# Optimization experiments

Measured on AMD Instinct MI355X. Metric: run time of the kernel, lower is better.

## Reference

```python
import jax, jax.numpy as jnp
import numpy as np

NUM_USERS = 100000
NUM_ITEMS = 100000
DIM = 128
B = 8192
H = 200
ATTN_HID = 64


def setup_inputs() -> dict:
    key = jax.random.key(0)
    ks = jax.random.split(key, 10)
    user_ids = jax.random.randint(ks[0], (B,), 0, NUM_USERS)
    item_ids = jax.random.randint(ks[1], (B,), 0, NUM_ITEMS)
    user_history = jax.random.randint(ks[2], (B, H), 0, NUM_ITEMS)
    user_table = jax.random.normal(ks[3], (NUM_USERS, DIM), dtype=jnp.float32)
    item_table = jax.random.normal(ks[4], (NUM_ITEMS, DIM), dtype=jnp.float32)
    feature_interaction = jax.random.normal(ks[5], (DIM, DIM), dtype=jnp.float32)
    # attention MLP: Linear(2*DIM, 64) -> ReLU -> Linear(64, 1) -> Sigmoid
    lim1 = 1.0 / np.sqrt(2 * DIM)
    w1 = jax.random.uniform(ks[6], (2 * DIM, ATTN_HID), minval=-lim1, maxval=lim1, dtype=jnp.float32)
    b1 = jax.random.uniform(ks[7], (ATTN_HID,), minval=-lim1, maxval=lim1, dtype=jnp.float32)
    lim2 = 1.0 / np.sqrt(ATTN_HID)
    w2 = jax.random.uniform(ks[8], (ATTN_HID, 1), minval=-lim2, maxval=lim2, dtype=jnp.float32)
    b2 = jax.random.uniform(ks[9], (1,), minval=-lim2, maxval=lim2, dtype=jnp.float32)
    return {
        "user_ids": user_ids,
        "item_ids": item_ids,
        "user_history": user_history,
        "user_table": user_table,
        "item_table": item_table,
        "feature_interaction": feature_interaction,
        "w1": w1,
        "b1": b1,
        "w2": w2,
        "b2": b2,
    }


def reference(user_ids, item_ids, user_history, user_table, item_table,
              feature_interaction, w1, b1, w2, b2):
    user_emb = user_table[user_ids]          # [B, D]
    item_emb = item_table[item_ids]          # [B, D]
    # bilinear interaction: (user_emb @ W) . item_emb, summed over D -> [B, 1]
    interaction = jnp.sum((user_emb @ feature_interaction) * item_emb, axis=1, keepdims=True)
    # attention-weighted history pooling
    history_emb = item_table[user_history]   # [B, H, D]
    u = jnp.broadcast_to(user_emb[:, None, :], history_emb.shape)  # [B, H, D]
    attn_in = jnp.concatenate([u, history_emb], axis=-1)           # [B, H, 2D]
    h = jax.nn.relu(attn_in @ w1 + b1)                             # [B, H, 64]
    attn_w = jax.nn.sigmoid(h @ w2 + b2)                           # [B, H, 1]
    history_repr = jnp.sum(attn_w * history_emb, axis=1)           # [B, D]
    user_out = user_emb + history_repr
    return (user_out, item_emb, interaction)
```

## Files before the change

kernel.cpp:

```cpp
#include <hip/hip_runtime.h>
#include <math.h>

#define NB      8192
#define HLEN    200
#define DIM     128
#define AH      64
#define NITEMS  100000
#define NTILE   13

typedef __attribute__((ext_vector_type(4))) float f32x4;
typedef __attribute__((ext_vector_type(2))) float f32x2;
typedef __attribute__((ext_vector_type(4))) int   i32x4;
typedef __attribute__((ext_vector_type(8))) short bf16x8;

__device__ __forceinline__ unsigned short f2bf(float f) {
  unsigned int u = __float_as_uint(f);
  u += 0x7fffu + ((u >> 16) & 1u);
  return (unsigned short)(u >> 16);
}
__device__ __forceinline__ float bf2f(unsigned short h) {
  return __uint_as_float(((unsigned int)h) << 16);
}
__device__ __forceinline__ long pick64(const i32x4& v, int h) {
  return (long)(unsigned)v[2 * h] | ((long)(unsigned)v[2 * h + 1] << 32);
}

__global__ void convert_kernel(const float* __restrict__ tbl,
                               const float* __restrict__ w1,
                               unsigned char* __restrict__ tbl8,
                               unsigned char* __restrict__ w1f8) {
  const long total4 = (long)NITEMS * DIM / 4;
  const long stride = (long)gridDim.x * blockDim.x;
  const long t0 = (long)blockIdx.x * blockDim.x + threadIdx.x;
  for (long i = t0; i < total4; i += stride) {
    f32x4 v = ((const f32x4*)tbl)[i];
    int p = __builtin_amdgcn_cvt_pk_fp8_f32(v[0], v[1], 0, false);
    p     = __builtin_amdgcn_cvt_pk_fp8_f32(v[2], v[3], p, true);
    ((int*)tbl8)[i] = p;
  }
  if (t0 < 16384) {
    int L = (int)t0;
    int j  = L & 7, gg = (L >> 3) & 3, mm = (L >> 5) & 15;
    int nt = (L >> 9) & 3, s = (L >> 11) & 3, part = (L >> 13) & 1;
    int kg = part * 128 + (s >> 1) * 64 + gg * 16 + (s & 1) * 8 + j;
    int n  = nt * 16 + mm;
    float v = w1[kg * AH + n];
    int p = __builtin_amdgcn_cvt_pk_fp8_f32(v, v, 0, false);
    w1f8[L] = (unsigned char)(p & 0xff);
  }
}

__global__ __launch_bounds__(256)
void main_kernel_fp8(const int* __restrict__ user_ids,
                     const int* __restrict__ user_history,
                     const float* __restrict__ user_table,
                     const unsigned char* __restrict__ tbl8,
                     const unsigned char* __restrict__ w1f8,
                     const float* __restrict__ b1,
                     const float* __restrict__ w2,
                     const float* __restrict__ b2,
                     float* __restrict__ out_user) {
  const int lane = threadIdx.x & 63;
  const int wave = threadIdx.x >> 6;
  const int b = blockIdx.x * 4 + wave;
  const int m = lane & 15;
  const int g = lane >> 4;

  const int uid = __builtin_amdgcn_readfirstlane(user_ids[b]);
  const float* urow = user_table + (long)uid * DIM;
  const int* hrow = user_history + (long)b * HLEN;

  int idxs[NTILE];
#pragma unroll
  for (int t = 0; t < NTILE; ++t) {
    int row = t * 16 + m;
    idxs[t] = (row < HLEN) ? hrow[row] : 0;
  }

  i32x4 uf[2];
#pragma unroll
  for (int kb = 0; kb < 2; ++kb) {
    const float* up = urow + kb * 64 + g * 16;
    f32x4 q0 = *(const f32x4*)(up + 0);
    f32x4 q1 = *(const f32x4*)(up + 4);
    f32x4 q2 = *(const f32x4*)(up + 8);
    f32x4 q3 = *(const f32x4*)(up + 12);
    i32x4 d;
    d[0] = __builtin_amdgcn_cvt_pk_fp8_f32(q0[0], q0[1], 0, false);
    d[0] = __builtin_amdgcn_cvt_pk_fp8_f32(q0[2], q0[3], d[0], true);
    d[1] = __builtin_amdgcn_cvt_pk_fp8_f32(q1[0], q1[1], 0, false);
    d[1] = __builtin_amdgcn_cvt_pk_fp8_f32(q1[2], q1[3], d[1], true);
    d[2] = __builtin_amdgcn_cvt_pk_fp8_f32(q2[0], q2[1], 0, false);
    d[2] = __builtin_amdgcn_cvt_pk_fp8_f32(q2[2], q2[3], d[2], true);
    d[3] = __builtin_amdgcn_cvt_pk_fp8_f32(q3[0], q3[1], 0, false);
    d[3] = __builtin_amdgcn_cvt_pk_fp8_f32(q3[2], q3[3], d[3], true);
    uf[kb] = d;
  }

  const unsigned char* wtop = w1f8;
  const unsigned char* wbot = w1f8 + 8192;

  f32x4 accu[4];
#pragma unroll
  for (int nt = 0; nt < 4; ++nt) accu[nt] = (f32x4){0.f, 0.f, 0.f, 0.f};
#pragma unroll
  for (int s = 0; s < 4; ++s) {
    long a_s = pick64(uf[s >> 1], s & 1);
#pragma unroll
    for (int nt = 0; nt < 4; ++nt) {
      long bf = *(const long*)(wtop + ((s * 4 + nt) * 16 + m) * 32 + g * 8);
      accu[nt] = __builtin_amdgcn_mfma_f32_16x16x32_fp8_fp8(a_s, bf, accu[nt], 0, 0, 0);
    }
  }
  float ubreg[4], w2reg[4];
#pragma unroll
  for (int nt = 0; nt < 4; ++nt) {
    ubreg[nt] = accu[nt][0] + b1[nt * 16 + m];
    w2reg[nt] = w2[nt * 16 + m];
  }
  const float b2v = b2[0];

  long bfr[4][4];
#pragma unroll
  for (int s = 0; s < 4; ++s)
#pragma unroll
    for (int nt = 0; nt < 4; ++nt)
      bfr[s][nt] = *(const long*)(wbot + ((s * 4 + nt) * 16 + m) * 32 + g * 8);

  float arep[32];
#pragma unroll
  for (int c = 0; c < 32; ++c) arep[c] = 0.f;

  i32x4 pa[3][2];
#define LOADT(T, BUF)                                                          \
  {                                                                            \
    const unsigned char* p_ = tbl8 + ((long)idxs[T] << 7) + g * 16;            \
    pa[BUF][0] = *(const i32x4*)p_;                                            \
    pa[BUF][1] = *(const i32x4*)(p_ + 64);                                     \
  }
  LOADT(0, 0)
  LOADT(1, 1)
#pragma unroll
  for (int t = 0; t < NTILE; ++t) {
    if (t + 2 < NTILE) LOADT(t + 2, (t + 2) % 3)
    const int cb = t % 3;

    f32x4 acc[4];
#pragma unroll
    for (int nt = 0; nt < 4; ++nt) acc[nt] = (f32x4){0.f, 0.f, 0.f, 0.f};
#pragma unroll
    for (int s = 0; s < 4; ++s) {
      long a_s = pick64(pa[cb][s >> 1], s & 1);
#pragma unroll
      for (int nt = 0; nt < 4; ++nt)
        acc[nt] = __builtin_amdgcn_mfma_f32_16x16x32_fp8_fp8(a_s, bfr[s][nt], acc[nt], 0, 0, 0);
    }

    float sums[4];
#pragma unroll
    for (int r = 0; r < 4; ++r) {
      float s = 0.f;
#pragma unroll
      for (int nt = 0; nt < 4; ++nt) {
        float h = fmaxf(acc[nt][r] + ubreg[nt], 0.f);
        s = fmaf(h, w2reg[nt], s);
      }
      s += __shfl_xor(s, 1);
      s += __shfl_xor(s, 2);
      s += __shfl_xor(s, 4);
      s += __shfl_xor(s, 8);
      sums[r] = s;
    }
    const int q = m & 3;
    float keep = (q == 0) ? sums[0] : (q == 1) ? sums[1] : (q == 2) ? sums[2] : sums[3];
    float sv = __shfl(keep, ((m >> 2) << 4) | m);
    float attw = 1.f / (1.f + __expf(-(sv + b2v)));
    if (t * 16 + m >= HLEN) attw = 0.f;

#pragma unroll
    for (int kb = 0; kb < 2; ++kb)
#pragma unroll
      for (int d = 0; d < 4; ++d) {
        f32x2 lo = __builtin_amdgcn_cvt_pk_f32_fp8(pa[cb][kb][d], false);
        f32x2 hi = __builtin_amdgcn_cvt_pk_f32_fp8(pa[cb][kb][d], true);
        const int base = kb * 16 + d * 4;
        arep[base + 0] = fmaf(attw, lo[0], arep[base + 0]);
        arep[base + 1] = fmaf(attw, lo[1], arep[base + 1]);
        arep[base + 2] = fmaf(attw, hi[0], arep[base + 2]);
        arep[base + 3] = fmaf(attw, hi[1], arep[base + 3]);
      }
  }
#undef LOADT

#pragma unroll
  for (int c = 0; c < 32; ++c) {
    arep[c] += __shfl_xor(arep[c], 1);
    arep[c] += __shfl_xor(arep[c], 2);
    arep[c] += __shfl_xor(arep[c], 4);
    arep[c] += __shfl_xor(arep[c], 8);
  }
  if (m == 0) {
#pragma unroll
    for (int kb = 0; kb < 2; ++kb)
#pragma unroll
      for (int i4 = 0; i4 < 4; ++i4) {
        const int col = kb * 64 + g * 16 + i4 * 4;
        f32x4 uv = *(const f32x4*)(urow + col);
        f32x4 o;
#pragma unroll
        for (int qq = 0; qq < 4; ++qq) o[qq] = uv[qq] + arep[kb * 16 + i4 * 4 + qq];
        *(f32x4*)(out_user + (long)b * DIM + col) = o;
      }
  }
}

__global__ __launch_bounds__(256)
void main_fallback(const int* __restrict__ user_ids,
                   const int* __restrict__ user_history,
                   const float* __restrict__ user_table,
                   const float* __restrict__ item_table,
                   const float* __restrict__ w1,
                   const float* __restrict__ b1,
                   const float* __restrict__ w2,
                   const float* __restrict__ b2,
                   float* __restrict__ out_user) {
  const int lane = threadIdx.x & 63;
  const int wave = threadIdx.x >> 6;
  const int b = blockIdx.x * 4 + wave;
  const int m = lane & 15, g = lane >> 4;
  const int uid = __builtin_amdgcn_readfirstlane(user_ids[b]);
  const float* urow = user_table + (long)uid * DIM;
  float upj = b1[lane];
#pragma unroll 8
  for (int d = 0; d < DIM; ++d) upj = fmaf(urow[d], w1[d * AH + lane], upj);
  bf16x8 bfr[4][4];
#pragma unroll
  for (int ks = 0; ks < 4; ++ks)
#pragma unroll
    for (int nt = 0; nt < 4; ++nt) {
      bf16x8 bv;
#pragma unroll
      for (int j = 0; j < 8; ++j)
        bv[j] = (short)f2bf(w1[(DIM + ks * 32 + g * 8 + j) * AH + nt * 16 + m]);
      bfr[ks][nt] = bv;
    }
  float ubreg[4], w2reg[4];
#pragma unroll
  for (int nt = 0; nt < 4; ++nt) {
    ubreg[nt] = __shfl(upj, nt * 16 + m);
    w2reg[nt] = w2[nt * 16 + m];
  }
  const float b2v = b2[0];
  float arep[32];
#pragma unroll
  for (int c = 0; c < 32; ++c) arep[c] = 0.f;
  const int* hrow = user_history + (long)b * HLEN;
  for (int t = 0; t < NTILE; ++t) {
    const int row = t * 16 + m;
    const int idx = (row < HLEN) ? hrow[row] : 0;
    bf16x8 a[4];
    const float* rp = item_table + (long)idx * DIM;
#pragma unroll
    for (int ks = 0; ks < 4; ++ks) {
      f32x4 lo = *(const f32x4*)(rp + ks * 32 + g * 8);
      f32x4 hi = *(const f32x4*)(rp + ks * 32 + g * 8 + 4);
      bf16x8 av;
      av[0] = (short)f2bf(lo[0]); av[1] = (short)f2bf(lo[1]);
      av[2] = (short)f2bf(lo[2]); av[3] = (short)f2bf(lo[3]);
      av[4] = (short)f2bf(hi[0]); av[5] = (short)f2bf(hi[1]);
      av[6] = (short)f2bf(hi[2]); av[7] = (short)f2bf(hi[3]);
      a[ks] = av;
    }
    f32x4 acc[4];
#pragma unroll
    for (int nt = 0; nt < 4; ++nt) acc[nt] = (f32x4){0.f, 0.f, 0.f, 0.f};
#pragma unroll
    for (int ks = 0; ks < 4; ++ks)
#pragma unroll
      for (int nt = 0; nt < 4; ++nt)
        acc[nt] = __builtin_amdgcn_mfma_f32_16x16x32_bf16(a[ks], bfr[ks][nt], acc[nt], 0, 0, 0);
    float sums[4];
#pragma unroll
    for (int r = 0; r < 4; ++r) {
      float s = 0.f;
#pragma unroll
      for (int nt = 0; nt < 4; ++nt) {
        float h = fmaxf(acc[nt][r] + ubreg[nt], 0.f);
        s = fmaf(h, w2reg[nt], s);
      }
      s += __shfl_xor(s, 1); s += __shfl_xor(s, 2);
      s += __shfl_xor(s, 4); s += __shfl_xor(s, 8);
      sums[r] = s;
    }
    const int q = m & 3;
    float keep = (q == 0) ? sums[0] : (q == 1) ? sums[1] : (q == 2) ? sums[2] : sums[3];
    float sv = __shfl(keep, ((m >> 2) << 4) | m);
    float attw = 1.f / (1.f + __expf(-(sv + b2v)));
    if (row >= HLEN) attw = 0.f;
#pragma unroll
    for (int ks = 0; ks < 4; ++ks)
#pragma unroll
      for (int j = 0; j < 8; ++j)
        arep[ks * 8 + j] = fmaf(attw, bf2f((unsigned short)a[ks][j]), arep[ks * 8 + j]);
  }
#pragma unroll
  for (int c = 0; c < 32; ++c) {
    arep[c] += __shfl_xor(arep[c], 1);
    arep[c] += __shfl_xor(arep[c], 2);
    arep[c] += __shfl_xor(arep[c], 4);
    arep[c] += __shfl_xor(arep[c], 8);
  }
  if (m == 0) {
#pragma unroll
    for (int ks = 0; ks < 4; ++ks)
#pragma unroll
      for (int j = 0; j < 8; ++j) {
        const int col = ks * 32 + g * 8 + j;
        out_user[(long)b * DIM + col] = urow[col] + arep[ks * 8 + j];
      }
  }
}

__global__ __launch_bounds__(256, 2)
void inter_kernel(const int* __restrict__ user_ids,
                  const int* __restrict__ item_ids,
                  const float* __restrict__ user_table,
                  const float* __restrict__ item_table,
                  const float* __restrict__ fi,
                  float* __restrict__ out_item,
                  float* __restrict__ out_inter) {
  __shared__ unsigned short fitb[DIM * 130];
  __shared__ float u4[4][DIM];
  __shared__ float red[4][4];
  const int t = threadIdx.x;
  for (int i = t; i < DIM * DIM; i += 256) {
    int d = i >> 7, e = i & 127;
    fitb[e * 130 + d] = f2bf(fi[i]);
  }
  const int col = t & 127;
  const int dh = t >> 7;
  const int lane = t & 63;
  const int wv = t >> 6;
  const int b0 = blockIdx.x * 32;
  const unsigned short* fr = &fitb[col * 130 + dh * 64];

  for (int grp = 0; grp < 8; ++grp) {
    __syncthreads();
    for (int i = t; i < 4 * DIM; i += 256) {
      int bi = i >> 7, d = i & 127;
      u4[bi][d] = user_table[(long)user_ids[b0 + grp * 4 + bi] * DIM + d];
    }
    __syncthreads();
    float a0 = 0.f, a1 = 0.f, a2 = 0.f, a3 = 0.f;
#pragma unroll 4
    for (int d = 0; d < 64; d += 4) {
      float f0 = bf2f(fr[d]), f1 = bf2f(fr[d + 1]), f2 = bf2f(fr[d + 2]), f3 = bf2f(fr[d + 3]);
      f32x4 q0 = *(const f32x4*)&u4[0][dh * 64 + d];
      f32x4 q1 = *(const f32x4*)&u4[1][dh * 64 + d];
      f32x4 q2 = *(const f32x4*)&u4[2][dh * 64 + d];
      f32x4 q3 = *(const f32x4*)&u4[3][dh * 64 + d];
      a0 = fmaf(f0, q0[0], a0); a0 = fmaf(f1, q0[1], a0); a0 = fmaf(f2, q0[2], a0); a0 = fmaf(f3, q0[3], a0);
      a1 = fmaf(f0, q1[0], a1); a1 = fmaf(f1, q1[1], a1); a1 = fmaf(f2, q1[2], a1); a1 = fmaf(f3, q1[3], a1);
      a2 = fmaf(f0, q2[0], a2); a2 = fmaf(f1, q2[1], a2); a2 = fmaf(f2, q2[2], a2); a2 = fmaf(f3, q2[3], a2);
      a3 = fmaf(f0, q3[0], a3); a3 = fmaf(f1, q3[1], a3); a3 = fmaf(f2, q3[2], a3); a3 = fmaf(f3, q3[3], a3);
    }
    const int bb = b0 + grp * 4;
    const float vv0 = item_table[(long)item_ids[bb + 0] * DIM + col];
    const float vv1 = item_table[(long)item_ids[bb + 1] * DIM + col];
    const float vv2 = item_table[(long)item_ids[bb + 2] * DIM + col];
    const float vv3 = item_table[(long)item_ids[bb + 3] * DIM + col];
    if (dh == 0) {
      out_item[(long)(bb + 0) * DIM + col] = vv0;
      out_item[(long)(bb + 1) * DIM + col] = vv1;
      out_item[(long)(bb + 2) * DIM + col] = vv2;
      out_item[(long)(bb + 3) * DIM + col] = vv3;
    }
    float p0 = a0 * vv0, p1 = a1 * vv1, p2 = a2 * vv2, p3 = a3 * vv3;
#pragma unroll
    for (int msk = 1; msk <= 32; msk <<= 1) {
      p0 += __shfl_xor(p0, msk);
      p1 += __shfl_xor(p1, msk);
      p2 += __shfl_xor(p2, msk);
      p3 += __shfl_xor(p3, msk);
    }
    if (lane == 0) { red[wv][0] = p0; red[wv][1] = p1; red[wv][2] = p2; red[wv][3] = p3; }
    __syncthreads();
    if (t < 4)
      out_inter[bb + t] = red[0][t] + red[1][t] + red[2][t] + red[3][t];
  }
}

extern "C" void kernel_launch(void* const* d_in, const int* in_sizes, int n_in,
                              void* d_out, int out_size, void* d_ws, size_t ws_size,
                              hipStream_t stream) {
  const int*   user_ids     = (const int*)d_in[0];
  const int*   item_ids     = (const int*)d_in[1];
  const int*   user_history = (const int*)d_in[2];
  const float* user_table   = (const float*)d_in[3];
  const float* item_table   = (const float*)d_in[4];
  const float* fi           = (const float*)d_in[5];
  const float* w1           = (const float*)d_in[6];
  const float* b1           = (const float*)d_in[7];
  const float* w2           = (const float*)d_in[8];
  const float* b2           = (const float*)d_in[9];

  float* out       = (float*)d_out;
  float* out_user  = out;
  float* out_item  = out + (size_t)NB * DIM;
  float* out_inter = out + (size_t)2 * NB * DIM;

  const size_t need = (size_t)NITEMS * DIM + 16384;
  if (ws_size >= need) {
    unsigned char* tbl8 = (unsigned char*)d_ws;
    unsigned char* w1f8 = tbl8 + (size_t)NITEMS * DIM;
    convert_kernel<<<1536, 256, 0, stream>>>(item_table, w1, tbl8, w1f8);
    main_kernel_fp8<<<NB / 4, 256, 0, stream>>>(user_ids, user_history, user_table,
        tbl8, w1f8, b1, w2, b2, out_user);
  } else {
    main_fallback<<<NB / 4, 256, 0, stream>>>(user_ids, user_history, user_table,
        item_table, w1, b1, w2, b2, out_user);
  }
  inter_kernel<<<NB / 32, 256, 0, stream>>>(user_ids, item_ids, user_table, item_table,
        fi, out_item, out_inter);
}
```

Measured before the change: 106.9 us.

## Merge interaction kernel into conversion kernel and deepen gather prefetch

```diff
diff --git a/kernel.cpp b/kernel.cpp
--- a/kernel.cpp
+++ b/kernel.cpp
@@ -7,46 +7,120 @@
 #define AH      64
 #define NITEMS  100000
 #define NTILE   13
+#define INTER_BLKS (NB / 32)
 
 typedef __attribute__((ext_vector_type(4))) float f32x4;
 typedef __attribute__((ext_vector_type(2))) float f32x2;
 typedef __attribute__((ext_vector_type(4))) int   i32x4;
 typedef __attribute__((ext_vector_type(8))) short bf16x8;
+typedef unsigned int uint;
 
 __device__ __forceinline__ unsigned short f2bf(float f) {
-  unsigned int u = __float_as_uint(f);
+  uint u = __float_as_uint(f);
   u += 0x7fffu + ((u >> 16) & 1u);
   return (unsigned short)(u >> 16);
 }
 __device__ __forceinline__ float bf2f(unsigned short h) {
-  return __uint_as_float(((unsigned int)h) << 16);
+  return __uint_as_float(((uint)h) << 16);
 }
 __device__ __forceinline__ long pick64(const i32x4& v, int h) {
   return (long)(unsigned)v[2 * h] | ((long)(unsigned)v[2 * h + 1] << 32);
 }
-
-__global__ void convert_kernel(const float* __restrict__ tbl,
-                               const float* __restrict__ w1,
-                               unsigned char* __restrict__ tbl8,
-                               unsigned char* __restrict__ w1f8) {
-  const long total4 = (long)NITEMS * DIM / 4;
-  const long stride = (long)gridDim.x * blockDim.x;
-  const long t0 = (long)blockIdx.x * blockDim.x + threadIdx.x;
-  for (long i = t0; i < total4; i += stride) {
-    f32x4 v = ((const f32x4*)tbl)[i];
-    int p = __builtin_amdgcn_cvt_pk_fp8_f32(v[0], v[1], 0, false);
-    p     = __builtin_amdgcn_cvt_pk_fp8_f32(v[2], v[3], p, true);
-    ((int*)tbl8)[i] = p;
-  }
-  if (t0 < 16384) {
-    int L = (int)t0;
-    int j  = L & 7, gg = (L >> 3) & 3, mm = (L >> 5) & 15;
-    int nt = (L >> 9) & 3, s = (L >> 11) & 3, part = (L >> 13) & 1;
-    int kg = part * 128 + (s >> 1) * 64 + gg * 16 + (s & 1) * 8 + j;
-    int n  = nt * 16 + mm;
-    float v = w1[kg * AH + n];
-    int p = __builtin_amdgcn_cvt_pk_fp8_f32(v, v, 0, false);
-    w1f8[L] = (unsigned char)(p & 0xff);
+__device__ __forceinline__ i32x4 ldnt(const void* p) {
+  return __builtin_nontemporal_load((const i32x4*)p);
+}
+
+__global__ __launch_bounds__(256)
+void pre_kernel(const int* __restrict__ user_ids,
+                const int* __restrict__ item_ids,
+                const float* __restrict__ user_table,
+                const float* __restrict__ item_table,
+                const float* __restrict__ fi,
+                const float* __restrict__ w1,
+                unsigned char* __restrict__ tbl8,
+                unsigned char* __restrict__ w1f8,
+                float* __restrict__ out_item,
+                float* __restrict__ out_inter) {
+  const int t = threadIdx.x;
+  if (blockIdx.x < INTER_BLKS) {
+    __shared__ unsigned short fitb[DIM * 130];
+    __shared__ float u4[4][DIM];
+    __shared__ float red[4][4];
+    for (int i = t; i < DIM * DIM; i += 256) {
+      int d = i >> 7, e = i & 127;
+      fitb[e * 130 + d] = f2bf(fi[i]);
+    }
+    const int col = t & 127;
+    const int dh = t >> 7;
+    const int lane = t & 63;
+    const int wv = t >> 6;
+    const int b0 = blockIdx.x * 32;
+    const unsigned short* fr = &fitb[col * 130 + dh * 64];
+    for (int grp = 0; grp < 8; ++grp) {
+      __syncthreads();
+      for (int i = t; i < 4 * DIM; i += 256) {
+        int bi = i >> 7, d = i & 127;
+        u4[bi][d] = user_table[(long)user_ids[b0 + grp * 4 + bi] * DIM + d];
+      }
+      __syncthreads();
+      float a0 = 0.f, a1 = 0.f, a2 = 0.f, a3 = 0.f;
+#pragma unroll 4
+      for (int d = 0; d < 64; d += 4) {
+        float f0 = bf2f(fr[d]), f1 = bf2f(fr[d + 1]), f2 = bf2f(fr[d + 2]), f3 = bf2f(fr[d + 3]);
+        f32x4 q0 = *(const f32x4*)&u4[0][dh * 64 + d];
+        f32x4 q1 = *(const f32x4*)&u4[1][dh * 64 + d];
+        f32x4 q2 = *(const f32x4*)&u4[2][dh * 64 + d];
+        f32x4 q3 = *(const f32x4*)&u4[3][dh * 64 + d];
+        a0 = fmaf(f0, q0[0], a0); a0 = fmaf(f1, q0[1], a0); a0 = fmaf(f2, q0[2], a0); a0 = fmaf(f3, q0[3], a0);
+        a1 = fmaf(f0, q1[0], a1); a1 = fmaf(f1, q1[1], a1); a1 = fmaf(f2, q1[2], a1); a1 = fmaf(f3, q1[3], a1);
+        a2 = fmaf(f0, q2[0], a2); a2 = fmaf(f1, q2[1], a2); a2 = fmaf(f2, q2[2], a2); a2 = fmaf(f3, q2[3], a2);
+        a3 = fmaf(f0, q3[0], a3); a3 = fmaf(f1, q3[1], a3); a3 = fmaf(f2, q3[2], a3); a3 = fmaf(f3, q3[3], a3);
+      }
+      const int bb = b0 + grp * 4;
+      const float vv0 = item_table[(long)item_ids[bb + 0] * DIM + col];
+      const float vv1 = item_table[(long)item_ids[bb + 1] * DIM + col];
+      const float vv2 = item_table[(long)item_ids[bb + 2] * DIM + col];
+      const float vv3 = item_table[(long)item_ids[bb + 3] * DIM + col];
+      if (dh == 0) {
+        out_item[(long)(bb + 0) * DIM + col] = vv0;
+        out_item[(long)(bb + 1) * DIM + col] = vv1;
+        out_item[(long)(bb + 2) * DIM + col] = vv2;
+        out_item[(long)(bb + 3) * DIM + col] = vv3;
+      }
+      float p0 = a0 * vv0, p1 = a1 * vv1, p2 = a2 * vv2, p3 = a3 * vv3;
+#pragma unroll
+      for (int msk = 1; msk <= 32; msk <<= 1) {
+        p0 += __shfl_xor(p0, msk);
+        p1 += __shfl_xor(p1, msk);
+        p2 += __shfl_xor(p2, msk);
+        p3 += __shfl_xor(p3, msk);
+      }
+      if (lane == 0) { red[wv][0] = p0; red[wv][1] = p1; red[wv][2] = p2; red[wv][3] = p3; }
+      __syncthreads();
+      if (t < 4)
+        out_inter[bb + t] = red[0][t] + red[1][t] + red[2][t] + red[3][t];
+    }
+  } else {
+    const int cb = blockIdx.x - INTER_BLKS;
+    const int cgrid = gridDim.x - INTER_BLKS;
+    const long t0 = (long)cb * 256 + t;
+    const long total4 = (long)NITEMS * DIM / 4;
+    const long stride = (long)cgrid * 256;
+    for (long i = t0; i < total4; i += stride) {
+      f32x4 v = ((const f32x4*)item_table)[i];
+      int p = __builtin_amdgcn_cvt_pk_fp8_f32(v[0], v[1], 0, false);
+      p     = __builtin_amdgcn_cvt_pk_fp8_f32(v[2], v[3], p, true);
+      ((int*)tbl8)[i] = p;
+    }
+    if (t0 < 16384) {
+      int L = (int)t0;
+      int j = L & 7, gg = (L >> 3) & 3, mm = (L >> 5) & 15;
+      int nt = (L >> 9) & 3, s = (L >> 11) & 3, part = (L >> 13) & 1;
+      int kg = part * 128 + (s >> 1) * 64 + gg * 16 + (s & 1) * 8 + j;
+      float v = w1[kg * AH + nt * 16 + mm];
+      int pk = __builtin_amdgcn_cvt_pk_fp8_f32(v, v, 0, false);
+      w1f8[L] = (unsigned char)(pk & 0xff);
+    }
   }
 }
 
@@ -76,6 +150,15 @@
     int row = t * 16 + m;
     idxs[t] = (row < HLEN) ? hrow[row] : 0;
   }
+
+  i32x4 pa[5][2];
+#define LOADT(T, BUF)                                                          \
+  {                                                                            \
+    const unsigned char* p_ = tbl8 + ((long)idxs[T] << 7) + g * 16;            \
+    pa[BUF][0] = ldnt(p_);                                                     \
+    pa[BUF][1] = ldnt(p_ + 64);                                                \
+  }
+  LOADT(0, 0) LOADT(1, 1) LOADT(2, 2) LOADT(3, 3)
 
   i32x4 uf[2];
 #pragma unroll
@@ -131,19 +214,10 @@
 #pragma unroll
   for (int c = 0; c < 32; ++c) arep[c] = 0.f;
 
-  i32x4 pa[3][2];
-#define LOADT(T, BUF)                                                          \
-  {                                                                            \
-    const unsigned char* p_ = tbl8 + ((long)idxs[T] << 7) + g * 16;            \
-    pa[BUF][0] = *(const i32x4*)p_;                                            \
-    pa[BUF][1] = *(const i32x4*)(p_ + 64);                                     \
-  }
-  LOADT(0, 0)
-  LOADT(1, 1)
 #pragma unroll
   for (int t = 0; t < NTILE; ++t) {
-    if (t + 2 < NTILE) LOADT(t + 2, (t + 2) % 3)
-    const int cb = t % 3;
+    if (t + 4 < NTILE) LOADT(t + 4, (t + 4) % 5)
+    const int cb = t % 5;
 
     f32x4 acc[4];
 #pragma unroll
@@ -321,75 +395,6 @@
   }
 }
 
-__global__ __launch_bounds__(256, 2)
-void inter_kernel(const int* __restrict__ user_ids,
-                  const int* __restrict__ item_ids,
-                  const float* __restrict__ user_table,
-                  const float* __restrict__ item_table,
-                  const float* __restrict__ fi,
-                  float* __restrict__ out_item,
-                  float* __restrict__ out_inter) {
-  __shared__ unsigned short fitb[DIM * 130];
-  __shared__ float u4[4][DIM];
-  __shared__ float red[4][4];
-  const int t = threadIdx.x;
-  for (int i = t; i < DIM * DIM; i += 256) {
-    int d = i >> 7, e = i & 127;
-    fitb[e * 130 + d] = f2bf(fi[i]);
-  }
-  const int col = t & 127;
-  const int dh = t >> 7;
-  const int lane = t & 63;
-  const int wv = t >> 6;
-  const int b0 = blockIdx.x * 32;
-  const unsigned short* fr = &fitb[col * 130 + dh * 64];
-
-  for (int grp = 0; grp < 8; ++grp) {
-    __syncthreads();
-    for (int i = t; i < 4 * DIM; i += 256) {
-      int bi = i >> 7, d = i & 127;
-      u4[bi][d] = user_table[(long)user_ids[b0 + grp * 4 + bi] * DIM + d];
-    }
-    __syncthreads();
-    float a0 = 0.f, a1 = 0.f, a2 = 0.f, a3 = 0.f;
-#pragma unroll 4
-    for (int d = 0; d < 64; d += 4) {
-      float f0 = bf2f(fr[d]), f1 = bf2f(fr[d + 1]), f2 = bf2f(fr[d + 2]), f3 = bf2f(fr[d + 3]);
-      f32x4 q0 = *(const f32x4*)&u4[0][dh * 64 + d];
-      f32x4 q1 = *(const f32x4*)&u4[1][dh * 64 + d];
-      f32x4 q2 = *(const f32x4*)&u4[2][dh * 64 + d];
-      f32x4 q3 = *(const f32x4*)&u4[3][dh * 64 + d];
-      a0 = fmaf(f0, q0[0], a0); a0 = fmaf(f1, q0[1], a0); a0 = fmaf(f2, q0[2], a0); a0 = fmaf(f3, q0[3], a0);
-      a1 = fmaf(f0, q1[0], a1); a1 = fmaf(f1, q1[1], a1); a1 = fmaf(f2, q1[2], a1); a1 = fmaf(f3, q1[3], a1);
-      a2 = fmaf(f0, q2[0], a2); a2 = fmaf(f1, q2[1], a2); a2 = fmaf(f2, q2[2], a2); a2 = fmaf(f3, q2[3], a2);
-      a3 = fmaf(f0, q3[0], a3); a3 = fmaf(f1, q3[1], a3); a3 = fmaf(f2, q3[2], a3); a3 = fmaf(f3, q3[3], a3);
-    }
-    const int bb = b0 + grp * 4;
-    const float vv0 = item_table[(long)item_ids[bb + 0] * DIM + col];
-    const float vv1 = item_table[(long)item_ids[bb + 1] * DIM + col];
-    const float vv2 = item_table[(long)item_ids[bb + 2] * DIM + col];
-    const float vv3 = item_table[(long)item_ids[bb + 3] * DIM + col];
-    if (dh == 0) {
-      out_item[(long)(bb + 0) * DIM + col] = vv0;
-      out_item[(long)(bb + 1) * DIM + col] = vv1;
-      out_item[(long)(bb + 2) * DIM + col] = vv2;
-      out_item[(long)(bb + 3) * DIM + col] = vv3;
-    }
-    float p0 = a0 * vv0, p1 = a1 * vv1, p2 = a2 * vv2, p3 = a3 * vv3;
-#pragma unroll
-    for (int msk = 1; msk <= 32; msk <<= 1) {
-      p0 += __shfl_xor(p0, msk);
-      p1 += __shfl_xor(p1, msk);
-      p2 += __shfl_xor(p2, msk);
-      p3 += __shfl_xor(p3, msk);
-    }
-    if (lane == 0) { red[wv][0] = p0; red[wv][1] = p1; red[wv][2] = p2; red[wv][3] = p3; }
-    __syncthreads();
-    if (t < 4)
-      out_inter[bb + t] = red[0][t] + red[1][t] + red[2][t] + red[3][t];
-  }
-}
-
 extern "C" void kernel_launch(void* const* d_in, const int* in_sizes, int n_in,
                               void* d_out, int out_size, void* d_ws, size_t ws_size,
                               hipStream_t stream) {
@@ -413,13 +418,14 @@
   if (ws_size >= need) {
     unsigned char* tbl8 = (unsigned char*)d_ws;
     unsigned char* w1f8 = tbl8 + (size_t)NITEMS * DIM;
-    convert_kernel<<<1536, 256, 0, stream>>>(item_table, w1, tbl8, w1f8);
+    pre_kernel<<<INTER_BLKS + 1024, 256, 0, stream>>>(user_ids, item_ids, user_table,
+        item_table, fi, w1, tbl8, w1f8, out_item, out_inter);
     main_kernel_fp8<<<NB / 4, 256, 0, stream>>>(user_ids, user_history, user_table,
         tbl8, w1f8, b1, w2, b2, out_user);
   } else {
     main_fallback<<<NB / 4, 256, 0, stream>>>(user_ids, user_history, user_table,
         item_table, w1, b1, w2, b2, out_user);
-  }
-  inter_kernel<<<NB / 32, 256, 0, stream>>>(user_ids, item_ids, user_table, item_table,
-        fi, out_item, out_inter);
-}
+    pre_kernel<<<INTER_BLKS, 256, 0, stream>>>(user_ids, item_ids, user_table,
+        item_table, fi, w1, nullptr, nullptr, out_item, out_inter);
+  }
+}
```

After: 109.1 us. 2.0% more time.
